# Kernel optimization log

Hardware: AMD Instinct MI355X
Metric: run time of the kernel (lower is better)

## Reference

```python
import jax, jax.numpy as jnp
import numpy as np

B, L, D = 128, 196, 512
T = 20
V, E, H, A = 10000, 256, 512, 512


def setup_inputs() -> dict:
    key = jax.random.key(0)
    ks = jax.random.split(key, 20)
    s = lambda *sh: 0.02
    inp = {
        "a": jax.random.normal(ks[0], (B, L, D), jnp.float32),
        "captions": jax.random.randint(ks[1], (B, T), 0, V),
        "lengths": jnp.full((B,), T, dtype=jnp.int64),
        "embed_W": jax.random.normal(ks[2], (V, E), jnp.float32) * 0.02,
        "Wa": jax.random.normal(ks[3], (D, A), jnp.float32) * 0.02,
        "Wh": jax.random.normal(ks[4], (H, A), jnp.float32) * 0.02,
        "Wc": jax.random.normal(ks[5], (H, A), jnp.float32) * 0.02,
        "v": jax.random.normal(ks[6], (A,), jnp.float32) * 0.02,
        "beta_W": jax.random.normal(ks[7], (H, 1), jnp.float32) * 0.02,
        "beta_b": jnp.zeros((1,), jnp.float32),
        "W_ih": jax.random.normal(ks[8], (E + D, 4 * H), jnp.float32) * 0.02,
        "W_hh": jax.random.normal(ks[9], (H, 4 * H), jnp.float32) * 0.02,
        "b_ih": jnp.zeros((4 * H,), jnp.float32),
        "b_hh": jnp.zeros((4 * H,), jnp.float32),
        "fc_W": jax.random.normal(ks[10], (H, V), jnp.float32) * 0.02,
        "fc_b": jnp.zeros((V,), jnp.float32),
        "initW_h": jax.random.normal(ks[11], (D, H), jnp.float32) * 0.02,
        "initb_h": jnp.zeros((H,), jnp.float32),
        "initW_c": jax.random.normal(ks[12], (D, H), jnp.float32) * 0.02,
        "initb_c": jnp.zeros((H,), jnp.float32),
    }
    return inp


def _decode(a, captions, embed_W, Wa, Wh, Wc, v, beta_W, beta_b,
            W_ih, W_hh, b_ih, b_hh, fc_W, fc_b,
            initW_h, initb_h, initW_c, initb_c):
    # dropout layers are treated as identity (eval mode) for a deterministic reference
    emb = embed_W[captions]                       # (B, T, E)
    mean_ctx = a.mean(axis=1)                     # (B, D)
    h0 = jnp.tanh(mean_ctx @ initW_h + initb_h)   # (B, H)
    c0 = jnp.tanh(mean_ctx @ initW_c + initb_c)
    wa = a @ Wa                                   # (B, L, A), hoisted (invariant over t)
    Hd = h0.shape[-1]

    def step(carry, x_t):
        h, c, prev_h = carry
        # dual additive attention: scores from annotations + h + prev_h (context_input)
        score = jnp.tanh(wa + (h @ Wh)[:, None, :] + (prev_h @ Wc)[:, None, :])  # (B,L,A)
        e = score @ v                                                            # (B,L)
        alpha = jax.nn.softmax(e, axis=1)
        beta = jax.nn.sigmoid(h @ beta_W + beta_b)                               # (B,1)
        ctx = beta * jnp.einsum('bl,bld->bd', alpha, a)                          # (B,D)
        # LSTMCell
        x = jnp.concatenate([x_t, ctx], axis=1)                                  # (B,E+D)
        gates = x @ W_ih + b_ih + h @ W_hh + b_hh                                # (B,4H)
        i, f, g, o = jnp.split(gates, 4, axis=1)
        c_new = jax.nn.sigmoid(f) * c + jax.nn.sigmoid(i) * jnp.tanh(g)
        h_new = jax.nn.sigmoid(o) * jnp.tanh(c_new)
        logits_t = h_new @ fc_W + fc_b                                           # (B,V)
        return (h_new, c_new, h_new), (logits_t, alpha)

    xs = jnp.swapaxes(emb[:, :T - 1, :], 0, 1)    # (T-1, B, E) time-major
    _, (logits_t, alphas_t) = jax.lax.scan(step, (h0, c0, h0), xs)
    # all lengths == T: pack_padded_sequence(batch_first=True).data is time-major flatten
    packed_logits = logits_t.reshape((T - 1) * a.shape[0], -1)                   # ((T-1)*B, V)
    alphas = jnp.swapaxes(alphas_t, 0, 1)                                        # (B, T-1, L)
    return packed_logits, alphas


def reference(a, captions, lengths, embed_W, Wa, Wh, Wc, v, beta_W, beta_b,
              W_ih, W_hh, b_ih, b_hh, fc_W, fc_b,
              initW_h, initb_h, initW_c, initb_c):
    return _decode(a, captions, embed_W, Wa, Wh, Wc, v, beta_W, beta_b,
                   W_ih, W_hh, b_ih, b_hh, fc_W, fc_b,
                   initW_h, initb_h, initW_c, initb_c)
```

## Files before the change

kernel.cpp:

```cpp
#include <hip/hip_runtime.h>
#include <hip/hip_bf16.h>
#include <math.h>

#define B_ 128
#define L_ 196
#define D_ 512
#define T_ 20
#define V_ 10000
#define E_ 256
#define H_ 512
#define A_ 512
#define TM1 19
#define ROWS (TM1*B_)
#define G4H 2048
#define KCAT 1024
#define LH 98

typedef unsigned short ushort_t;
typedef __attribute__((ext_vector_type(8))) short bf16x8;
typedef __attribute__((ext_vector_type(4))) float f32x4;

__device__ __forceinline__ float fast_tanh(float x){
    float ax = fabsf(x);
    float e = __expf(-2.f*ax);
    float r = __builtin_amdgcn_rcpf(1.f + e);
    return copysignf((1.f - e)*r, x);
}
__device__ __forceinline__ float sigmoidf_(float x){
    return __builtin_amdgcn_rcpf(1.f + __expf(-x));
}
__device__ __forceinline__ ushort_t f2b(float f){
    union{float f; unsigned u;} x; x.f = f;
    unsigned r = x.u + 0x7fffu + ((x.u>>16)&1u);
    return (ushort_t)(r>>16);
}
__device__ __forceinline__ float b2f(ushort_t h){
    union{unsigned u; float f;} x; x.u = ((unsigned)h)<<16;
    return x.f;
}
__device__ __forceinline__ float b2f_lo(unsigned u){ union{unsigned u; float f;} x; x.u = u<<16; return x.f; }
__device__ __forceinline__ float b2f_hi(unsigned u){ union{unsigned u; float f;} x; x.u = u & 0xffff0000u; return x.f; }

template<int OUT_BF16, int HAS_BIAS, int NT, int SWZ>
__global__ __launch_bounds__(256)
void gemm_mfma(const ushort_t* __restrict__ A, int lda,
               const ushort_t* __restrict__ BT, int ldb,
               void* __restrict__ Cout, int ldc,
               int N, int K, const float* __restrict__ bias)
{
// ... 135 lines not shown
struct TJob { const float* src; const float* src2; ushort_t* dst;
              int lds, Ksz, Nsz, koff, ldk, nx, nblk; };
struct TJobs { TJob j[6]; };

__global__ __launch_bounds__(256) void combo_trans_k(TJobs J){
    __shared__ float t[32][33];
    int bid = blockIdx.x;
    int ji = 0;
    while (bid >= J.j[ji].nblk){ bid -= J.j[ji].nblk; ji++; }
    const TJob jb = J.j[ji];
    int n0 = (bid % jb.nx)*32, k0 = (bid / jb.nx)*32;
    int tx = threadIdx.x & 31, ty = threadIdx.x >> 5;
    #pragma unroll
    for (int kk = ty; kk < 32; kk += 8){
        int k = k0 + kk, n = n0 + tx;
        float v = 0.f;
        if (k < jb.Ksz && n < jb.Nsz){
            v = jb.src[(size_t)k*jb.lds + n];
            if (jb.src2) v += jb.src2[(size_t)k*jb.lds + n];
        }
        t[kk][tx] = v;
    }
    __syncthreads();
    #pragma unroll
    for (int nn = ty; nn < 32; nn += 8){
        int n = n0 + nn, k = k0 + tx;
        if (k < jb.Ksz) jb.dst[(size_t)n*jb.ldk + jb.koff + k] = f2b(t[tx][nn]);
    }
}

__global__ __launch_bounds__(256) void mean_cvt_k(const float* __restrict__ a, ushort_t* __restrict__ a_b,
                                                  float* __restrict__ mc,
                                                  const float* __restrict__ b_ih, const float* __restrict__ b_hh,
                                                  float* __restrict__ bias4h, unsigned* __restrict__ ebar){
    if (blockIdx.x == 256){
        for (int k = threadIdx.x; k < G4H; k += 256) bias4h[k] = b_ih[k] + b_hh[k];
        if (threadIdx.x < B_) ebar[threadIdx.x] = 0u;
        return;
    }
    int idx = blockIdx.x*256 + threadIdx.x;
    int b = idx >> 9, d = idx & 511;
    const float* p = a + (size_t)b*L_*D_ + d;
    ushort_t* q = a_b + (size_t)b*L_*D_ + d;
    float s = 0.f;
    for (int l=0;l<L_;l++){ float v = p[(size_t)l*D_]; s += v; q[(size_t)l*D_] = f2b(v); }
    mc[idx] = s * (1.f/(float)L_);
}

__global__ void gather_emb(const int* __restrict__ captions, const float* __restrict__ embW,
                           ushort_t* __restrict__ xemb){
    int i = blockIdx.x;
    int t = i / B_, b = i - t*B_;
    int cap = captions[b*T_ + t];
    float4 v = ((const float4*)(embW + (size_t)cap*E_))[threadIdx.x];
    ushort_t r[4] = {f2b(v.x),f2b(v.y),f2b(v.z),f2b(v.w)};
    *(uint2*)(xemb + (size_t)i*E_ + threadIdx.x*4) = *(uint2*)r;
}

__global__ __launch_bounds__(512) void hw0cvt_k(const float* __restrict__ h0f,
                        const ushort_t* __restrict__ WhcT,
                        ushort_t* __restrict__ xcat, float* __restrict__ hWp){
    int b = blockIdx.x, tid = threadIdx.x;
    int lane = tid & 63, wave = tid >> 6;
    __shared__ ushort_t hls[512];
    float hv = h0f[b*H_ + tid];
    ushort_t hb = f2b(hv);
    xcat[(size_t)b*KCAT + D_ + tid] = hb;
    hls[tid] = hb;
    hWp[(size_t)(b*2+1)*512 + tid] = 0.f;
    __syncthreads();
    int wn = wave * 64;
    int col16 = lane & 15;
    int khi = (lane >> 4) * 8;
    bool a_on = (col16 == 0);
    f32x4 acc[4];
    #pragma unroll
    for (int f=0;f<4;f++) acc[f] = (f32x4){0.f,0.f,0.f,0.f};
    for (int kk=0; kk<16; kk++){
        bf16x8 af = (bf16x8){0,0,0,0,0,0,0,0};
        if (a_on) af = *(const bf16x8*)&hls[kk*32 + khi];
        #pragma unroll
        for (int f=0;f<4;f++){
            bf16x8 bf = *(const bf16x8*)(WhcT + (size_t)(wn + f*16 + col16)*512 + kk*32 + khi);
            acc[f] = __builtin_amdgcn_mfma_f32_16x16x32_bf16(af, bf, acc[f], 0, 0, 0);
        }
    }
    if (lane < 16){
        #pragma unroll
        for (int f=0;f<4;f++) hWp[(size_t)(b*2+0)*512 + wn + f*16 + lane] = acc[f][0];
    }
}

__global__ __launch_bounds__(512) void mega2_k(const ushort_t* __restrict__ wa,
                        const ushort_t* __restrict__ a_b,
                        const float* __restrict__ v,
                        const float* __restrict__ beta_W, const float* __restrict__ beta_b,
                        const ushort_t* __restrict__ WhcT,
                        const float* __restrict__ gp, const float* __restrict__ embWih,
                        float* __restrict__ cbuf, float* __restrict__ hWp,
                        ushort_t* __restrict__ xcat, ushort_t* __restrict__ Hall,
                        float* __restrict__ alphas_out, float* __restrict__ ebuf,
                        unsigned* __restrict__ ebar, int t)
{
    const int b = blockIdx.x, half = blockIdx.y;
    const int tid = threadIdx.x;
    const int lane = tid & 63, wave = tid >> 6;
    __shared__ ushort_t hls[256];
    __shared__ float red[512];
    __shared__ float al_s[224];
    __shared__ float part[2][256];

    if (t > 0){
        if (tid < 256){
            const int j = half*256 + tid;
            const float* eb = embWih + ((size_t)((t-1)*B_ + b))*G4H;
            float gi = eb[j], gf = eb[H_+j], gg = eb[2*H_+j], go = eb[3*H_+j];
            #pragma unroll
            for (int ks=0; ks<8; ks++){
                const float* g = gp + ((size_t)(ks*B_ + b))*G4H;
                gi += g[j]; gf += g[H_+j]; gg += g[2*H_+j]; go += g[3*H_+j];
            }
            float ig = sigmoidf_(gi), fg = sigmoidf_(gf);
            float g2 = fast_tanh(gg), og = sigmoidf_(go);
            float c = fg*cbuf[b*H_+j] + ig*g2;
            float h = og*fast_tanh(c);
            cbuf[b*H_+j] = c;
            ushort_t hb = f2b(h);
            xcat[(size_t)b*KCAT + D_ + j] = hb;
            Hall[((size_t)(t-1)*B_ + b)*H_ + j] = hb;
            hls[tid] = hb;
        }
        __syncthreads();
        int wn = wave * 64;
        int col16 = lane & 15;
        int khi = (lane >> 4) * 8;
        bool a_on = (col16 == 0);
        f32x4 acc[4];
        #pragma unroll
        for (int f=0;f<4;f++) acc[f] = (f32x4){0.f,0.f,0.f,0.f};
        #pragma unroll
        for (int kk=0; kk<8; kk++){
            bf16x8 af = (bf16x8){0,0,0,0,0,0,0,0};
            if (a_on) af = *(const bf16x8*)&hls[kk*32 + khi];
            #pragma unroll
            for (int f=0;f<4;f++){
                bf16x8 bf = *(const bf16x8*)(WhcT + (size_t)(wn + f*16 + col16)*512 + half*256 + kk*32 + khi);
                acc[f] = __builtin_amdgcn_mfma_f32_16x16x32_bf16(af, bf, acc[f], 0, 0, 0);
            }
        }
        if (lane < 16){
            #pragma unroll
            for (int f=0;f<4;f++) hWp[(size_t)(b*2+half)*512 + wn + f*16 + lane] = acc[f][0];
        }
    }
    __syncthreads();
    if (tid == 0){
        __threadfence();
        atomicAdd(&ebar[b], 1u);
        const unsigned tgt = 2u*(unsigned)(2*t+1);
        while (__hip_atomic_load(&ebar[b], __ATOMIC_ACQUIRE, __HIP_MEMORY_SCOPE_AGENT) < tgt)
            __builtin_amdgcn_s_sleep(1);
    }
    __syncthreads();
    {
        const float* hp0 = hWp + (size_t)(b*2+0)*512 + lane*8;
        const float* hp1 = hWp + (size_t)(b*2+1)*512 + lane*8;
        float4 p00 = *(const float4*)hp0, p01 = *(const float4*)(hp0+4);
        float4 p10 = *(const float4*)hp1, p11 = *(const float4*)(hp1+4);
        float4 hw0 = make_float4(p00.x+p10.x, p00.y+p10.y, p00.z+p10.z, p00.w+p10.w);
        float4 hw1 = make_float4(p01.x+p11.x, p01.y+p11.y, p01.z+p11.z, p01.w+p11.w);
        const float* vp = v + lane*8;
        float4 v0 = *(const float4*)vp, v1 = *(const float4*)(vp+4);
        const int l0 = half*LH;
        for (int r = wave; r < LH; r += 8){
            int4 raw = *(const int4*)(wa + (((size_t)(b*L_ + l0 + r))<<9) + lane*8);
            const unsigned* u = (const unsigned*)&raw;
            float s;
            s  = fast_tanh(b2f_lo(u[0]) + hw0.x)*v0.x;
            s += fast_tanh(b2f_hi(u[0]) + hw0.y)*v0.y;
            s += fast_tanh(b2f_lo(u[1]) + hw0.z)*v0.z;
            s += fast_tanh(b2f_hi(u[1]) + hw0.w)*v0.w;
            s += fast_tanh(b2f_lo(u[2]) + hw1.x)*v1.x;
            s += fast_tanh(b2f_hi(u[2]) + hw1.y)*v1.y;
            s += fast_tanh(b2f_lo(u[3]) + hw1.z)*v1.z;
            s += fast_tanh(b2f_hi(u[3]) + hw1.w)*v1.w;
            #pragma unroll
            for (int off=32; off; off>>=1) s += __shfl_down(s, off);
            if (lane==0) ebuf[b*L_ + l0 + r] = s;
        }
    }
    __syncthreads();
    if (tid == 0){
        __threadfence();
        atomicAdd(&ebar[b], 1u);
        const unsigned tgt = 2u*(unsigned)(2*t+2);
        while (__hip_atomic_load(&ebar[b], __ATOMIC_ACQUIRE, __HIP_MEMORY_SCOPE_AGENT) < tgt)
            __builtin_amdgcn_s_sleep(1);
    }
    __syncthreads();
    float ev = (tid < L_) ? ebuf[b*L_ + tid] : -3.0e38f;
    red[tid] = ev; __syncthreads();
    #pragma unroll
    for (int s=256; s; s>>=1){ if (tid<s) red[tid] = fmaxf(red[tid], red[tid+s]); __syncthreads(); }
    float m = red[0]; __syncthreads();
    float pr = (tid < L_) ? __expf(ev - m) : 0.f;
    red[tid] = pr; __syncthreads();
    #pragma unroll
    for (int s=256; s; s>>=1){ if (tid<s) red[tid] += red[tid+s]; __syncthreads(); }
    float inv = 1.f / red[0];
    __syncthreads();
    if (tid < L_) al_s[tid] = pr*inv;
    const int l0 = half*LH;
    if (tid >= l0 && tid < l0 + LH)
        __builtin_nontemporal_store(pr*inv, alphas_out + (size_t)b*TM1*L_ + (size_t)t*L_ + tid);
    float dv = b2f(xcat[(size_t)b*KCAT + D_ + tid]) * beta_W[tid];
    red[tid] = dv; __syncthreads();
    #pragma unroll
    for (int s=256; s; s>>=1){ if (tid<s) red[tid] += red[tid+s]; __syncthreads(); }
    float beta = sigmoidf_(red[0] + beta_b[0]);
    __syncthreads();
    const int d  = half*256 + (tid & 255);
    const int lr = tid >> 8;
    const ushort_t* pa = a_b + (((size_t)(b*L_ + lr*LH))<<9) + d;
    float s0 = 0.f;
    #pragma unroll 7
    for (int i=0; i<LH; ++i) s0 = fmaf(al_s[lr*LH + i], b2f(pa[(size_t)i*512]), s0);
    part[lr][tid & 255] = s0;
    __syncthreads();
    if (tid < 256)
        xcat[(size_t)b*KCAT + half*256 + tid] = f2b(beta*(part[0][tid] + part[1][tid]));
}

__global__ __launch_bounds__(256) void gates_k(const ushort_t* __restrict__ xcat,
                        const ushort_t* __restrict__ WcatT, float* __restrict__ gp){
    __shared__ ushort_t As[128*32];
    __shared__ ushort_t Bs[64*32];
    const int bn = blockIdx.x*64;
    const int ks = blockIdx.y;
    const int tid = threadIdx.x;
    const int lane = tid & 63, wave = tid >> 6;
    const int wm = wave*32;
    const int lrow = lane & 15;
    const int lk8 = (lane >> 4) * 8;
    f32x4 acc[2][4];
    #pragma unroll
    for (int i=0;i<2;i++)
        #pragma unroll
        for (int j=0;j<4;j++) acc[i][j] = (f32x4){0.f,0.f,0.f,0.f};

    for (int kk = 0; kk < 4; ++kk){
        int k0 = ks*128 + kk*32;
        int c0 = 2*tid;
        int r0 = c0 >> 2,  kq0 = (c0 & 3)*8;
        int r1 = (c0+1) >> 2, kq1 = ((c0+1) & 3)*8;
        int4 a0 = *(const int4*)(xcat + (size_t)r0*KCAT + k0 + kq0);
        int4 a1 = *(const int4*)(xcat + (size_t)r1*KCAT + k0 + kq1);
        int rb = tid >> 2, kqb = (tid & 3)*8;
        int4 b0 = *(const int4*)(WcatT + (size_t)(bn+rb)*KCAT + k0 + kqb);
        __syncthreads();
        *(int4*)&As[r0*32 + kq0] = a0;
        *(int4*)&As[r1*32 + kq1] = a1;
        *(int4*)&Bs[rb*32 + kqb] = b0;
        __syncthreads();
        bf16x8 af[2], bfr[4];
        #pragma unroll
        for (int i=0;i<2;i++) af[i] = *(bf16x8*)&As[(wm + i*16 + lrow)*32 + lk8];
        #pragma unroll
        for (int j=0;j<4;j++) bfr[j] = *(bf16x8*)&Bs[(j*16 + lrow)*32 + lk8];
        #pragma unroll
        for (int i=0;i<2;i++)
            #pragma unroll
            for (int j=0;j<4;j++)
                acc[i][j] = __builtin_amdgcn_mfma_f32_16x16x32_bf16(af[i], bfr[j], acc[i][j], 0, 0, 0);
    }
    const int rq = (lane >> 4) * 4;
    #pragma unroll
    for (int i=0;i<2;i++){
        #pragma unroll
        for (int j=0;j<4;j++){
            int gcol = bn + j*16 + lrow;
            #pragma unroll
            for (int q=0;q<4;q++){
                int grow = wm + i*16 + rq + q;
                gp[((size_t)(ks*B_ + grow))*G4H + gcol] = acc[i][j][q];
            }
        }
    }
}

__global__ __launch_bounds__(512) void lstmfin_k(const float* __restrict__ gp, const float* __restrict__ embWih,
                       const float* __restrict__ cbuf, ushort_t* __restrict__ Hall){
    int b = blockIdx.x, j = threadIdx.x;
    const float* eb = embWih + ((size_t)(18*B_ + b))*G4H;
    float gi = eb[j], gf = eb[H_+j], gg = eb[2*H_+j], go = eb[3*H_+j];
    #pragma unroll
    for (int ks=0; ks<8; ks++){
        const float* g = gp + ((size_t)(ks*B_ + b))*G4H;
        gi += g[j]; gf += g[H_+j]; gg += g[2*H_+j]; go += g[3*H_+j];
    }
    float ig = sigmoidf_(gi), fg = sigmoidf_(gf);
    float g2 = fast_tanh(gg), og = sigmoidf_(go);
    float c = fg*cbuf[b*H_+j] + ig*g2;
    float h = og*fast_tanh(c);
    Hall[((size_t)18*B_ + b)*H_ + j] = f2b(h);
}

extern "C" void kernel_launch(void* const* d_in, const int* in_sizes, int n_in,
                              void* d_out, int out_size, void* d_ws, size_t ws_size,
                              hipStream_t stream) {
    const float* a      = (const float*)d_in[0];
    const int*   caps   = (const int*)  d_in[1];
    const float* embW   = (const float*)d_in[3];
    const float* Wa     = (const float*)d_in[4];
    const float* Wh     = (const float*)d_in[5];
    const float* Wc     = (const float*)d_in[6];
    const float* v      = (const float*)d_in[7];
    const float* beta_W = (const float*)d_in[8];
    const float* beta_b = (const float*)d_in[9];
    const float* W_ih   = (const float*)d_in[10];
    const float* W_hh   = (const float*)d_in[11];
    const float* b_ih   = (const float*)d_in[12];
    const float* b_hh   = (const float*)d_in[13];
    const float* fc_W   = (const float*)d_in[14];
    const float* fc_b   = (const float*)d_in[15];
    const float* iWh    = (const float*)d_in[16];
    const float* ibh    = (const float*)d_in[17];
    const float* iWc    = (const float*)d_in[18];
    const float* ibc    = (const float*)d_in[19];

    float* out    = (float*)d_out;
    float* alphas = out + (size_t)ROWS*V_;

    char* ob = (char*)d_out;
    ushort_t* wa_b   = (ushort_t*)(ob);
    ushort_t* a_b    = (ushort_t*)(ob + 25690112);
    float*    embWih = (float*)   (ob + 51380224);

    char* wb = (char*)d_ws;
    float* mean_ctx = (float*)(wb);
    float* cbuf     = (float*)(wb + 262144);
    float* h0f      = (float*)(wb + 524288);
    float* hWp      = (float*)(wb + 786432);
    float* ebuf     = (float*)(wb + 1310720);
    float* bias4h   = (float*)(wb + 1413120);
    unsigned* ebar  = (unsigned*)(wb + 1421312);
    float* gp       = (float*)(wb + 1422336);
    ushort_t* xcat_b = (ushort_t*)(wb + 9810944);
    ushort_t* xemb_b = (ushort_t*)(wb + 10073088);
    ushort_t* Hall   = (ushort_t*)(wb + 11318272);
    ushort_t* WaT    = (ushort_t*)(wb + 13808640);
    ushort_t* WhcT   = (ushort_t*)(wb + 14332928);
    ushort_t* WihT   = (ushort_t*)(wb + 14857216);
    ushort_t* WcatT  = (ushort_t*)(wb + 15905792);
    ushort_t* fcWT   = (ushort_t*)(wb + 20100096);

    TJobs J;
    J.j[0] = { Wa,   nullptr, WaT,  512, 512, 512,  0,   512,  16, 256 };
    J.j[1] = { Wh,   Wc,      WhcT, 512, 512, 512,  0,   512,  16, 256 };
    J.j[2] = { W_ih, nullptr, WihT, G4H, 256, G4H,  0,   256,  64, 512 };
    J.j[3] = { W_ih + (size_t)E_*G4H, nullptr, WcatT, G4H, 512, G4H, 0,   KCAT, 64, 1024 };
    J.j[4] = { W_hh, nullptr, WcatT, G4H, 512, G4H,  512, KCAT, 64, 1024 };
    J.j[5] = { fc_W, nullptr, fcWT, V_,  512, V_,   0,   512,  316, 5056 };
    combo_trans_k<<<8128, 256, 0, stream>>>(J);
    mean_cvt_k<<<257, 256, 0, stream>>>(a, a_b, mean_ctx, b_ih, b_hh, bias4h, ebar);
    gather_emb<<<ROWS, 64, 0, stream>>>(caps, embW, xemb_b);
    gemm64t2<<<dim3(8,2,2), 256, 0, stream>>>(mean_ctx, D_, iWh, iWc, H_, h0f, cbuf, H_, ibh, ibc);
    hw0cvt_k<<<B_, 512, 0, stream>>>(h0f, WhcT, xcat_b, hWp);
    gemm_mfma<1,0,0,0><<<dim3(4,196), 256, 0, stream>>>(a_b, D_, WaT, D_, wa_b, A_, A_, D_, nullptr);
    gemm_mfma<0,1,0,0><<<dim3(16,19), 256, 0, stream>>>(xemb_b, E_, WihT, E_, embWih, G4H, G4H, E_, bias4h);

    for (int t = 0; t < TM1; ++t){
        mega2_k<<<dim3(B_,2), 512, 0, stream>>>(wa_b, a_b, v, beta_W, beta_b, WhcT,
                                                gp, embWih, cbuf, hWp, xcat_b, Hall,
                                                alphas, ebuf, ebar, t);
        gates_k<<<dim3(32,8), 256, 0, stream>>>(xcat_b, WcatT, gp);
    }
    lstmfin_k<<<B_, 512, 0, stream>>>(gp, embWih, cbuf, Hall);

    gemm_mfma<0,1,1,1><<<dim3(1520), 256, 0, stream>>>(Hall, H_, fcWT, H_, out, V_, V_, H_, fc_b);
}
```

Before: 1.054 ms.

## Fuse per-timestep attention and gate kernels into one persistent cooperative kernel

Replaces the 19 pairs of per-timestep launches (attention kernel plus gates GEMM) and the final LSTM kernel with a single cooperative persistent kernel of 256 blocks. Timesteps are separated by global atomic spin barriers instead of kernel boundaries. The gates GEMM is retiled to fit 512-thread blocks. This removes about 39 launch gaps and their drain/fill overhead, at the cost of grid-wide barriers with sleep polling and a fixed 256-block residency requirement.

```diff
diff --git a/kernel.cpp b/kernel.cpp
--- a/kernel.cpp
+++ b/kernel.cpp
@@ -15,6 +15,7 @@
 #define G4H 2048
 #define KCAT 1024
 #define LH 98
+#define NBLK 256
 
 typedef unsigned short ushort_t;
 typedef __attribute__((ext_vector_type(8))) short bf16x8;
@@ -216,10 +217,10 @@
 __global__ __launch_bounds__(256) void mean_cvt_k(const float* __restrict__ a, ushort_t* __restrict__ a_b,
                                                   float* __restrict__ mc,
                                                   const float* __restrict__ b_ih, const float* __restrict__ b_hh,
-                                                  float* __restrict__ bias4h, unsigned* __restrict__ ebar){
+                                                  float* __restrict__ bias4h, unsigned* __restrict__ bars){
     if (blockIdx.x == 256){
         for (int k = threadIdx.x; k < G4H; k += 256) bias4h[k] = b_ih[k] + b_hh[k];
-        if (threadIdx.x < B_) ebar[threadIdx.x] = 0u;
+        if (threadIdx.x < B_ + 1) bars[threadIdx.x] = 0u;
         return;
     }
     int idx = blockIdx.x*256 + threadIdx.x;
@@ -275,218 +276,220 @@
     }
 }
 
-__global__ __launch_bounds__(512) void mega2_k(const ushort_t* __restrict__ wa,
-                        const ushort_t* __restrict__ a_b,
-                        const float* __restrict__ v,
-                        const float* __restrict__ beta_W, const float* __restrict__ beta_b,
-                        const ushort_t* __restrict__ WhcT,
-                        const float* __restrict__ gp, const float* __restrict__ embWih,
-                        float* __restrict__ cbuf, float* __restrict__ hWp,
-                        ushort_t* __restrict__ xcat, ushort_t* __restrict__ Hall,
-                        float* __restrict__ alphas_out, float* __restrict__ ebuf,
-                        unsigned* __restrict__ ebar, int t)
-{
-    const int b = blockIdx.x, half = blockIdx.y;
+struct LoopArgs {
+    const ushort_t* wa;
+    const ushort_t* a_b;
+    const float* v;
+    const float* beta_W;
+    const float* beta_b;
+    const ushort_t* WhcT;
+    const ushort_t* WcatT;
+    const float* embWih;
+    float* cbuf;
+    float* hWp;
+    ushort_t* xcat;
+    ushort_t* Hall;
+    float* alphas;
+    float* ebuf;
+    float* gp;
+    unsigned* ebar;
+    unsigned* gbar;
+};
+
+__device__ __forceinline__ void spin_sync(unsigned* ctr, unsigned tgt){
+    __syncthreads();
+    if (threadIdx.x == 0){
+        __threadfence();
+        atomicAdd(ctr, 1u);
+        while (__hip_atomic_load(ctr, __ATOMIC_ACQUIRE, __HIP_MEMORY_SCOPE_AGENT) < tgt)
+            __builtin_amdgcn_s_sleep(1);
+    }
+    __syncthreads();
+}
+
+__global__ __launch_bounds__(512) void loop2_k(LoopArgs p){
+    const int blk = blockIdx.x;
+    const int b = blk >> 1, half = blk & 1;
     const int tid = threadIdx.x;
     const int lane = tid & 63, wave = tid >> 6;
     __shared__ ushort_t hls[256];
     __shared__ float red[512];
     __shared__ float al_s[224];
     __shared__ float part[2][256];
-
-    if (t > 0){
-        if (tid < 256){
-            const int j = half*256 + tid;
-            const float* eb = embWih + ((size_t)((t-1)*B_ + b))*G4H;
-            float gi = eb[j], gf = eb[H_+j], gg = eb[2*H_+j], go = eb[3*H_+j];
-            #pragma unroll
-            for (int ks=0; ks<8; ks++){
-                const float* g = gp + ((size_t)(ks*B_ + b))*G4H;
-                gi += g[j]; gf += g[H_+j]; gg += g[2*H_+j]; go += g[3*H_+j];
-            }
-            float ig = sigmoidf_(gi), fg = sigmoidf_(gf);
-            float g2 = fast_tanh(gg), og = sigmoidf_(go);
-            float c = fg*cbuf[b*H_+j] + ig*g2;
-            float h = og*fast_tanh(c);
-            cbuf[b*H_+j] = c;
-            ushort_t hb = f2b(h);
-            xcat[(size_t)b*KCAT + D_ + j] = hb;
-            Hall[((size_t)(t-1)*B_ + b)*H_ + j] = hb;
-            hls[tid] = hb;
-        }
-        __syncthreads();
-        int wn = wave * 64;
-        int col16 = lane & 15;
-        int khi = (lane >> 4) * 8;
-        bool a_on = (col16 == 0);
-        f32x4 acc[4];
-        #pragma unroll
-        for (int f=0;f<4;f++) acc[f] = (f32x4){0.f,0.f,0.f,0.f};
-        #pragma unroll
-        for (int kk=0; kk<8; kk++){
-            bf16x8 af = (bf16x8){0,0,0,0,0,0,0,0};
-            if (a_on) af = *(const bf16x8*)&hls[kk*32 + khi];
-            #pragma unroll
-            for (int f=0;f<4;f++){
-                bf16x8 bf = *(const bf16x8*)(WhcT + (size_t)(wn + f*16 + col16)*512 + half*256 + kk*32 + khi);
-                acc[f] = __builtin_amdgcn_mfma_f32_16x16x32_bf16(af, bf, acc[f], 0, 0, 0);
-            }
-        }
-        if (lane < 16){
-            #pragma unroll
-            for (int f=0;f<4;f++) hWp[(size_t)(b*2+half)*512 + wn + f*16 + lane] = acc[f][0];
-        }
-    }
-    __syncthreads();
-    if (tid == 0){
-        __threadfence();
-        atomicAdd(&ebar[b], 1u);
-        const unsigned tgt = 2u*(unsigned)(2*t+1);
-        while (__hip_atomic_load(&ebar[b], __ATOMIC_ACQUIRE, __HIP_MEMORY_SCOPE_AGENT) < tgt)
-            __builtin_amdgcn_s_sleep(1);
-    }
-    __syncthreads();
-    {
-        const float* hp0 = hWp + (size_t)(b*2+0)*512 + lane*8;
-        const float* hp1 = hWp + (size_t)(b*2+1)*512 + lane*8;
-        float4 p00 = *(const float4*)hp0, p01 = *(const float4*)(hp0+4);
-        float4 p10 = *(const float4*)hp1, p11 = *(const float4*)(hp1+4);
-        float4 hw0 = make_float4(p00.x+p10.x, p00.y+p10.y, p00.z+p10.z, p00.w+p10.w);
-        float4 hw1 = make_float4(p01.x+p11.x, p01.y+p11.y, p01.z+p11.z, p01.w+p11.w);
-        const float* vp = v + lane*8;
-        float4 v0 = *(const float4*)vp, v1 = *(const float4*)(vp+4);
-        const int l0 = half*LH;
-        for (int r = wave; r < LH; r += 8){
-            int4 raw = *(const int4*)(wa + (((size_t)(b*L_ + l0 + r))<<9) + lane*8);
-            const unsigned* u = (const unsigned*)&raw;
-            float s;
-            s  = fast_tanh(b2f_lo(u[0]) + hw0.x)*v0.x;
-            s += fast_tanh(b2f_hi(u[0]) + hw0.y)*v0.y;
-            s += fast_tanh(b2f_lo(u[1]) + hw0.z)*v0.z;
-            s += fast_tanh(b2f_hi(u[1]) + hw0.w)*v0.w;
-            s += fast_tanh(b2f_lo(u[2]) + hw1.x)*v1.x;
-            s += fast_tanh(b2f_hi(u[2]) + hw1.y)*v1.y;
-            s += fast_tanh(b2f_lo(u[3]) + hw1.z)*v1.z;
-            s += fast_tanh(b2f_hi(u[3]) + hw1.w)*v1.w;
-            #pragma unroll
-            for (int off=32; off; off>>=1) s += __shfl_down(s, off);
-            if (lane==0) ebuf[b*L_ + l0 + r] = s;
-        }
-    }
-    __syncthreads();
-    if (tid == 0){
-        __threadfence();
-        atomicAdd(&ebar[b], 1u);
-        const unsigned tgt = 2u*(unsigned)(2*t+2);
-        while (__hip_atomic_load(&ebar[b], __ATOMIC_ACQUIRE, __HIP_MEMORY_SCOPE_AGENT) < tgt)
-            __builtin_amdgcn_s_sleep(1);
-    }
-    __syncthreads();
-    float ev = (tid < L_) ? ebuf[b*L_ + tid] : -3.0e38f;
-    red[tid] = ev; __syncthreads();
-    #pragma unroll
-    for (int s=256; s; s>>=1){ if (tid<s) red[tid] = fmaxf(red[tid], red[tid+s]); __syncthreads(); }
-    float m = red[0]; __syncthreads();
-    float pr = (tid < L_) ? __expf(ev - m) : 0.f;
-    red[tid] = pr; __syncthreads();
-    #pragma unroll
-    for (int s=256; s; s>>=1){ if (tid<s) red[tid] += red[tid+s]; __syncthreads(); }
-    float inv = 1.f / red[0];
-    __syncthreads();
-    if (tid < L_) al_s[tid] = pr*inv;
-    const int l0 = half*LH;
-    if (tid >= l0 && tid < l0 + LH)
-        __builtin_nontemporal_store(pr*inv, alphas_out + (size_t)b*TM1*L_ + (size_t)t*L_ + tid);
-    float dv = b2f(xcat[(size_t)b*KCAT + D_ + tid]) * beta_W[tid];
-    red[tid] = dv; __syncthreads();
-    #pragma unroll
-    for (int s=256; s; s>>=1){ if (tid<s) red[tid] += red[tid+s]; __syncthreads(); }
-    float beta = sigmoidf_(red[0] + beta_b[0]);
-    __syncthreads();
-    const int d  = half*256 + (tid & 255);
-    const int lr = tid >> 8;
-    const ushort_t* pa = a_b + (((size_t)(b*L_ + lr*LH))<<9) + d;
-    float s0 = 0.f;
-    #pragma unroll 7
-    for (int i=0; i<LH; ++i) s0 = fmaf(al_s[lr*LH + i], b2f(pa[(size_t)i*512]), s0);
-    part[lr][tid & 255] = s0;
-    __syncthreads();
-    if (tid < 256)
-        xcat[(size_t)b*KCAT + half*256 + tid] = f2b(beta*(part[0][tid] + part[1][tid]));
-}
-
-__global__ __launch_bounds__(256) void gates_k(const ushort_t* __restrict__ xcat,
-                        const ushort_t* __restrict__ WcatT, float* __restrict__ gp){
     __shared__ ushort_t As[128*32];
     __shared__ ushort_t Bs[64*32];
-    const int bn = blockIdx.x*64;
-    const int ks = blockIdx.y;
-    const int tid = threadIdx.x;
-    const int lane = tid & 63, wave = tid >> 6;
-    const int wm = wave*32;
-    const int lrow = lane & 15;
-    const int lk8 = (lane >> 4) * 8;
-    f32x4 acc[2][4];
-    #pragma unroll
-    for (int i=0;i<2;i++)
-        #pragma unroll
-        for (int j=0;j<4;j++) acc[i][j] = (f32x4){0.f,0.f,0.f,0.f};
-
-    for (int kk = 0; kk < 4; ++kk){
-        int k0 = ks*128 + kk*32;
-        int c0 = 2*tid;
-        int r0 = c0 >> 2,  kq0 = (c0 & 3)*8;
-        int r1 = (c0+1) >> 2, kq1 = ((c0+1) & 3)*8;
-        int4 a0 = *(const int4*)(xcat + (size_t)r0*KCAT + k0 + kq0);
-        int4 a1 = *(const int4*)(xcat + (size_t)r1*KCAT + k0 + kq1);
-        int rb = tid >> 2, kqb = (tid & 3)*8;
-        int4 b0 = *(const int4*)(WcatT + (size_t)(bn+rb)*KCAT + k0 + kqb);
-        __syncthreads();
-        *(int4*)&As[r0*32 + kq0] = a0;
-        *(int4*)&As[r1*32 + kq1] = a1;
-        *(int4*)&Bs[rb*32 + kqb] = b0;
-        __syncthreads();
-        bf16x8 af[2], bfr[4];
-        #pragma unroll
-        for (int i=0;i<2;i++) af[i] = *(bf16x8*)&As[(wm + i*16 + lrow)*32 + lk8];
-        #pragma unroll
-        for (int j=0;j<4;j++) bfr[j] = *(bf16x8*)&Bs[(j*16 + lrow)*32 + lk8];
-        #pragma unroll
-        for (int i=0;i<2;i++)
-            #pragma unroll
-            for (int j=0;j<4;j++)
-                acc[i][j] = __builtin_amdgcn_mfma_f32_16x16x32_bf16(af[i], bfr[j], acc[i][j], 0, 0, 0);
-    }
-    const int rq = (lane >> 4) * 4;
-    #pragma unroll
-    for (int i=0;i<2;i++){
-        #pragma unroll
-        for (int j=0;j<4;j++){
-            int gcol = bn + j*16 + lrow;
-            #pragma unroll
-            for (int q=0;q<4;q++){
-                int grow = wm + i*16 + rq + q;
-                gp[((size_t)(ks*B_ + grow))*G4H + gcol] = acc[i][j][q];
+    unsigned gtgt = 0;
+
+    for (int t = 0; t < TM1; ++t){
+        if (t > 0){
+            if (tid < 256){
+                const int j = half*256 + tid;
+                const float* eb = p.embWih + ((size_t)((t-1)*B_ + b))*G4H;
+                float gi = eb[j], gf = eb[H_+j], gg = eb[2*H_+j], go = eb[3*H_+j];
+                #pragma unroll
+                for (int ks=0; ks<8; ks++){
+                    const float* g = p.gp + ((size_t)(ks*B_ + b))*G4H;
+                    gi += g[j]; gf += g[H_+j]; gg += g[2*H_+j]; go += g[3*H_+j];
+                }
+                float ig = sigmoidf_(gi), fg = sigmoidf_(gf);
+                float g2 = fast_tanh(gg), og = sigmoidf_(go);
+                float c = fg*p.cbuf[b*H_+j] + ig*g2;
+                float h = og*fast_tanh(c);
+                p.cbuf[b*H_+j] = c;
+                ushort_t hb = f2b(h);
+                p.xcat[(size_t)b*KCAT + D_ + j] = hb;
+                p.Hall[((size_t)(t-1)*B_ + b)*H_ + j] = hb;
+                hls[tid] = hb;
             }
-        }
-    }
-}
-
-__global__ __launch_bounds__(512) void lstmfin_k(const float* __restrict__ gp, const float* __restrict__ embWih,
-                       const float* __restrict__ cbuf, ushort_t* __restrict__ Hall){
-    int b = blockIdx.x, j = threadIdx.x;
-    const float* eb = embWih + ((size_t)(18*B_ + b))*G4H;
-    float gi = eb[j], gf = eb[H_+j], gg = eb[2*H_+j], go = eb[3*H_+j];
-    #pragma unroll
-    for (int ks=0; ks<8; ks++){
-        const float* g = gp + ((size_t)(ks*B_ + b))*G4H;
-        gi += g[j]; gf += g[H_+j]; gg += g[2*H_+j]; go += g[3*H_+j];
-    }
-    float ig = sigmoidf_(gi), fg = sigmoidf_(gf);
-    float g2 = fast_tanh(gg), og = sigmoidf_(go);
-    float c = fg*cbuf[b*H_+j] + ig*g2;
-    float h = og*fast_tanh(c);
-    Hall[((size_t)18*B_ + b)*H_ + j] = f2b(h);
+            __syncthreads();
+            int wn = wave * 64;
+            int col16 = lane & 15;
+            int khi = (lane >> 4) * 8;
+            bool a_on = (col16 == 0);
+            f32x4 acc[4];
+            #pragma unroll
+            for (int f=0;f<4;f++) acc[f] = (f32x4){0.f,0.f,0.f,0.f};
+            #pragma unroll
+            for (int kk=0; kk<8; kk++){
+                bf16x8 af = (bf16x8){0,0,0,0,0,0,0,0};
+                if (a_on) af = *(const bf16x8*)&hls[kk*32 + khi];
+                #pragma unroll
+                for (int f=0;f<4;f++){
+                    bf16x8 bf = *(const bf16x8*)(p.WhcT + (size_t)(wn + f*16 + col16)*512 + half*256 + kk*32 + khi);
+                    acc[f] = __builtin_amdgcn_mfma_f32_16x16x32_bf16(af, bf, acc[f], 0, 0, 0);
+                }
+            }
+            if (lane < 16){
+                #pragma unroll
+                for (int f=0;f<4;f++) p.hWp[(size_t)(b*2+half)*512 + wn + f*16 + lane] = acc[f][0];
+            }
+        }
+        spin_sync(&p.ebar[b], 4u*(unsigned)t + 2u);
+        {
+            const float* hp0 = p.hWp + (size_t)(b*2+0)*512 + lane*8;
+            const float* hp1 = p.hWp + (size_t)(b*2+1)*512 + lane*8;
+            float4 p00 = *(const float4*)hp0, p01 = *(const float4*)(hp0+4);
+            float4 p10 = *(const float4*)hp1, p11 = *(const float4*)(hp1+4);
+            float4 hw0 = make_float4(p00.x+p10.x, p00.y+p10.y, p00.z+p10.z, p00.w+p10.w);
+            float4 hw1 = make_float4(p01.x+p11.x, p01.y+p11.y, p01.z+p11.z, p01.w+p11.w);
+            const float* vp = p.v + lane*8;
+            float4 v0 = *(const float4*)vp, v1 = *(const float4*)(vp+4);
+            const int l0 = half*LH;
+            for (int r = wave; r < LH; r += 8){
+                int4 raw = *(const int4*)(p.wa + (((size_t)(b*L_ + l0 + r))<<9) + lane*8);
+                const unsigned* u = (const unsigned*)&raw;
+                float s;
+                s  = fast_tanh(b2f_lo(u[0]) + hw0.x)*v0.x;
+                s += fast_tanh(b2f_hi(u[0]) + hw0.y)*v0.y;
+                s += fast_tanh(b2f_lo(u[1]) + hw0.z)*v0.z;
+                s += fast_tanh(b2f_hi(u[1]) + hw0.w)*v0.w;
+                s += fast_tanh(b2f_lo(u[2]) + hw1.x)*v1.x;
+                s += fast_tanh(b2f_hi(u[2]) + hw1.y)*v1.y;
+                s += fast_tanh(b2f_lo(u[3]) + hw1.z)*v1.z;
+                s += fast_tanh(b2f_hi(u[3]) + hw1.w)*v1.w;
+                #pragma unroll
+                for (int off=32; off; off>>=1) s += __shfl_down(s, off);
+                if (lane==0) p.ebuf[b*L_ + l0 + r] = s;
+            }
+        }
+        spin_sync(&p.ebar[b], 4u*(unsigned)t + 4u);
+        {
+            float ev = (tid < L_) ? p.ebuf[b*L_ + tid] : -3.0e38f;
+            red[tid] = ev; __syncthreads();
+            #pragma unroll
+            for (int s=256; s; s>>=1){ if (tid<s) red[tid] = fmaxf(red[tid], red[tid+s]); __syncthreads(); }
+            float m = red[0]; __syncthreads();
+            float pr = (tid < L_) ? __expf(ev - m) : 0.f;
+            red[tid] = pr; __syncthreads();
+            #pragma unroll
+            for (int s=256; s; s>>=1){ if (tid<s) red[tid] += red[tid+s]; __syncthreads(); }
+            float inv = 1.f / red[0];
+            __syncthreads();
+            if (tid < L_) al_s[tid] = pr*inv;
+            const int l0 = half*LH;
+            if (tid >= l0 && tid < l0 + LH)
+                __builtin_nontemporal_store(pr*inv, p.alphas + (size_t)b*TM1*L_ + (size_t)t*L_ + tid);
+            float dv = b2f(p.xcat[(size_t)b*KCAT + D_ + tid]) * p.beta_W[tid];
+            red[tid] = dv; __syncthreads();
+            #pragma unroll
+            for (int s=256; s; s>>=1){ if (tid<s) red[tid] += red[tid+s]; __syncthreads(); }
+            float beta = sigmoidf_(red[0] + p.beta_b[0]);
+            __syncthreads();
+            const int d  = half*256 + (tid & 255);
+            const int lr = tid >> 8;
+            const ushort_t* pa = p.a_b + (((size_t)(b*L_ + lr*LH))<<9) + d;
+            float s0 = 0.f;
+            #pragma unroll 7
+            for (int i=0; i<LH; ++i) s0 = fmaf(al_s[lr*LH + i], b2f(pa[(size_t)i*512]), s0);
+            part[lr][tid & 255] = s0;
+            __syncthreads();
+            if (tid < 256)
+                p.xcat[(size_t)b*KCAT + half*256 + tid] = f2b(beta*(part[0][tid] + part[1][tid]));
+        }
+        gtgt += NBLK; spin_sync(p.gbar, gtgt);
+        {
+            const int bn = (blk & 31) * 64;
+            const int ks = blk >> 5;
+            const int wm = (wave & 3) * 32;
+            const int wn = (wave >> 2) * 32;
+            const int lrow = lane & 15, lk8 = (lane >> 4) * 8;
+            const int ra = tid >> 2, kqa = (tid & 3)*8;
+            f32x4 acc[2][2];
+            #pragma unroll
+            for (int i=0;i<2;i++)
+                #pragma unroll
+                for (int j=0;j<2;j++) acc[i][j] = (f32x4){0.f,0.f,0.f,0.f};
+            #pragma unroll
+            for (int kk = 0; kk < 4; ++kk){
+                int k0 = ks*128 + kk*32;
+                int4 av = *(const int4*)(p.xcat + (size_t)ra*KCAT + k0 + kqa);
+                int4 bv;
+                if (tid < 256) bv = *(const int4*)(p.WcatT + (size_t)(bn + ra)*KCAT + k0 + kqa);
+                __syncthreads();
+                *(int4*)&As[ra*32 + kqa] = av;
+                if (tid < 256) *(int4*)&Bs[ra*32 + kqa] = bv;
+                __syncthreads();
+                bf16x8 af[2], bfr[2];
+                #pragma unroll
+                for (int i=0;i<2;i++) af[i]  = *(bf16x8*)&As[(wm + i*16 + lrow)*32 + lk8];
+                #pragma unroll
+                for (int j=0;j<2;j++) bfr[j] = *(bf16x8*)&Bs[(wn + j*16 + lrow)*32 + lk8];
+                #pragma unroll
+                for (int i=0;i<2;i++)
+                    #pragma unroll
+                    for (int j=0;j<2;j++)
+                        acc[i][j] = __builtin_amdgcn_mfma_f32_16x16x32_bf16(af[i], bfr[j], acc[i][j], 0, 0, 0);
+            }
+            const int rq = (lane >> 4) * 4;
+            #pragma unroll
+            for (int i=0;i<2;i++)
+                #pragma unroll
+                for (int j=0;j<2;j++){
+                    int gcol = bn + wn + j*16 + lrow;
+                    #pragma unroll
+                    for (int q=0;q<4;q++){
+                        int grow = wm + i*16 + rq + q;
+                        p.gp[((size_t)(ks*B_ + grow))*G4H + gcol] = acc[i][j][q];
+                    }
+                }
+        }
+        gtgt += NBLK; spin_sync(p.gbar, gtgt);
+    }
+    if (tid < 256){
+        const int j = half*256 + tid;
+        const float* eb = p.embWih + ((size_t)(18*B_ + b))*G4H;
+        float gi = eb[j], gf = eb[H_+j], gg = eb[2*H_+j], go = eb[3*H_+j];
+        #pragma unroll
+        for (int ks=0; ks<8; ks++){
+            const float* g = p.gp + ((size_t)(ks*B_ + b))*G4H;
+            gi += g[j]; gf += g[H_+j]; gg += g[2*H_+j]; go += g[3*H_+j];
+        }
+        float ig = sigmoidf_(gi), fg = sigmoidf_(gf);
+        float g2 = fast_tanh(gg), og = sigmoidf_(go);
+        float c = fg*p.cbuf[b*H_+j] + ig*g2;
+        float h = og*fast_tanh(c);
+        p.Hall[((size_t)18*B_ + b)*H_ + j] = f2b(h);
+    }
 }
 
 extern "C" void kernel_launch(void* const* d_in, const int* in_sizes, int n_in,
@@ -527,7 +530,7 @@
     float* hWp      = (float*)(wb + 786432);
     float* ebuf     = (float*)(wb + 1310720);
     float* bias4h   = (float*)(wb + 1413120);
-    unsigned* ebar  = (unsigned*)(wb + 1421312);
+    unsigned* bars  = (unsigned*)(wb + 1421312);
     float* gp       = (float*)(wb + 1422336);
     ushort_t* xcat_b = (ushort_t*)(wb + 9810944);
     ushort_t* xemb_b = (ushort_t*)(wb + 10073088);
@@ -546,20 +549,21 @@
     J.j[4] = { W_hh, nullptr, WcatT, G4H, 512, G4H,  512, KCAT, 64, 1024 };
     J.j[5] = { fc_W, nullptr, fcWT, V_,  512, V_,   0,   512,  316, 5056 };
     combo_trans_k<<<8128, 256, 0, stream>>>(J);
-    mean_cvt_k<<<257, 256, 0, stream>>>(a, a_b, mean_ctx, b_ih, b_hh, bias4h, ebar);
+    mean_cvt_k<<<257, 256, 0, stream>>>(a, a_b, mean_ctx, b_ih, b_hh, bias4h, bars);
     gather_emb<<<ROWS, 64, 0, stream>>>(caps, embW, xemb_b);
     gemm64t2<<<dim3(8,2,2), 256, 0, stream>>>(mean_ctx, D_, iWh, iWc, H_, h0f, cbuf, H_, ibh, ibc);
     hw0cvt_k<<<B_, 512, 0, stream>>>(h0f, WhcT, xcat_b, hWp);
     gemm_mfma<1,0,0,0><<<dim3(4,196), 256, 0, stream>>>(a_b, D_, WaT, D_, wa_b, A_, A_, D_, nullptr);
     gemm_mfma<0,1,0,0><<<dim3(16,19), 256, 0, stream>>>(xemb_b, E_, WihT, E_, embWih, G4H, G4H, E_, bias4h);
 
-    for (int t = 0; t < TM1; ++t){
-        mega2_k<<<dim3(B_,2), 512, 0, stream>>>(wa_b, a_b, v, beta_W, beta_b, WhcT,
-                                                gp, embWih, cbuf, hWp, xcat_b, Hall,
-                                                alphas, ebuf, ebar, t);
-        gates_k<<<dim3(32,8), 256, 0, stream>>>(xcat_b, WcatT, gp);
-    }
-    lstmfin_k<<<B_, 512, 0, stream>>>(gp, embWih, cbuf, Hall);
+    LoopArgs la;
+    la.wa = wa_b; la.a_b = a_b; la.v = v; la.beta_W = beta_W; la.beta_b = beta_b;
+    la.WhcT = WhcT; la.WcatT = WcatT; la.embWih = embWih;
+    la.cbuf = cbuf; la.hWp = hWp; la.xcat = xcat_b; la.Hall = Hall;
+    la.alphas = alphas; la.ebuf = ebuf; la.gp = gp;
+    la.ebar = bars; la.gbar = bars + 128;
+    void* kargs[] = { &la };
+    hipLaunchCooperativeKernel((const void*)loop2_k, dim3(NBLK), dim3(512), kargs, 0, stream);
 
     gemm_mfma<0,1,1,1><<<dim3(1520), 256, 0, stream>>>(Hall, H_, fcWT, H_, out, V_, V_, H_, fc_b);
 }
```

Result: slower. 2.202 ms (+108.8%).

## Split per-step attention kernel into four quarter blocks per batch row

Applied to the files above, without the earlier changes.

The per-timestep attention/LSTM-cell kernel now runs as 4 blocks of 256 threads per batch element instead of 2 blocks of 512. The hW partial products are kept in four slices and summed after a cross-block spin barrier, which is factored into a helper, and the score rows and context columns are divided into quarters. Separately, mean_cvt is vectorized with float4 loads and gather_emb packs four rows per block. The aim is more, smaller blocks for better CU occupancy on the latency-bound recurrent loop, at the cost of more blocks spinning on each per-batch barrier and more redundant softmax/beta work.

```diff
diff --git a/kernel.cpp b/kernel.cpp
--- a/kernel.cpp
+++ b/kernel.cpp
@@ -14,7 +14,7 @@
 #define ROWS (TM1*B_)
 #define G4H 2048
 #define KCAT 1024
-#define LH 98
+#define LQ 49
 
 typedef unsigned short ushort_t;
 typedef __attribute__((ext_vector_type(8))) short bf16x8;
@@ -216,29 +216,37 @@
 __global__ __launch_bounds__(256) void mean_cvt_k(const float* __restrict__ a, ushort_t* __restrict__ a_b,
                                                   float* __restrict__ mc,
                                                   const float* __restrict__ b_ih, const float* __restrict__ b_hh,
-                                                  float* __restrict__ bias4h, unsigned* __restrict__ ebar){
-    if (blockIdx.x == 256){
+                                                  float* __restrict__ bias4h, unsigned* __restrict__ bars){
+    if (blockIdx.x == 64){
         for (int k = threadIdx.x; k < G4H; k += 256) bias4h[k] = b_ih[k] + b_hh[k];
-        if (threadIdx.x < B_) ebar[threadIdx.x] = 0u;
+        if (threadIdx.x < B_) bars[threadIdx.x] = 0u;
         return;
     }
     int idx = blockIdx.x*256 + threadIdx.x;
-    int b = idx >> 9, d = idx & 511;
-    const float* p = a + (size_t)b*L_*D_ + d;
-    ushort_t* q = a_b + (size_t)b*L_*D_ + d;
-    float s = 0.f;
-    for (int l=0;l<L_;l++){ float v = p[(size_t)l*D_]; s += v; q[(size_t)l*D_] = f2b(v); }
-    mc[idx] = s * (1.f/(float)L_);
-}
-
-__global__ void gather_emb(const int* __restrict__ captions, const float* __restrict__ embW,
+    int b = idx >> 7, dq = (idx & 127) * 4;
+    const float* p = a + (size_t)b*L_*D_ + dq;
+    ushort_t* q = a_b + (size_t)b*L_*D_ + dq;
+    float4 s = make_float4(0.f,0.f,0.f,0.f);
+    for (int l=0;l<L_;l++){
+        float4 v = *(const float4*)(p + (size_t)l*D_);
+        s.x += v.x; s.y += v.y; s.z += v.z; s.w += v.w;
+        ushort_t r[4] = {f2b(v.x),f2b(v.y),f2b(v.z),f2b(v.w)};
+        *(uint2*)(q + (size_t)l*D_) = *(uint2*)r;
+    }
+    const float inv = 1.f/(float)L_;
+    float4 o = make_float4(s.x*inv, s.y*inv, s.z*inv, s.w*inv);
+    *(float4*)(mc + (size_t)b*D_ + dq) = o;
+}
+
+__global__ __launch_bounds__(256) void gather_emb(const int* __restrict__ captions, const float* __restrict__ embW,
                            ushort_t* __restrict__ xemb){
-    int i = blockIdx.x;
+    int i = blockIdx.x*4 + (threadIdx.x >> 6);
+    int lane = threadIdx.x & 63;
     int t = i / B_, b = i - t*B_;
     int cap = captions[b*T_ + t];
-    float4 v = ((const float4*)(embW + (size_t)cap*E_))[threadIdx.x];
+    float4 v = ((const float4*)(embW + (size_t)cap*E_))[lane];
     ushort_t r[4] = {f2b(v.x),f2b(v.y),f2b(v.z),f2b(v.w)};
-    *(uint2*)(xemb + (size_t)i*E_ + threadIdx.x*4) = *(uint2*)r;
+    *(uint2*)(xemb + (size_t)i*E_ + lane*4) = *(uint2*)r;
 }
 
 __global__ __launch_bounds__(512) void hw0cvt_k(const float* __restrict__ h0f,
@@ -251,7 +259,9 @@
     ushort_t hb = f2b(hv);
     xcat[(size_t)b*KCAT + D_ + tid] = hb;
     hls[tid] = hb;
-    hWp[(size_t)(b*2+1)*512 + tid] = 0.f;
+    hWp[(size_t)(b*4+1)*512 + tid] = 0.f;
+    hWp[(size_t)(b*4+2)*512 + tid] = 0.f;
+    hWp[(size_t)(b*4+3)*512 + tid] = 0.f;
     __syncthreads();
     int wn = wave * 64;
     int col16 = lane & 15;
@@ -271,11 +281,22 @@
     }
     if (lane < 16){
         #pragma unroll
-        for (int f=0;f<4;f++) hWp[(size_t)(b*2+0)*512 + wn + f*16 + lane] = acc[f][0];
-    }
-}
-
-__global__ __launch_bounds__(512) void mega2_k(const ushort_t* __restrict__ wa,
+        for (int f=0;f<4;f++) hWp[(size_t)(b*4+0)*512 + wn + f*16 + lane] = acc[f][0];
+    }
+}
+
+__device__ __forceinline__ void spin_sync(unsigned* ctr, unsigned tgt){
+    __syncthreads();
+    if (threadIdx.x == 0){
+        __threadfence();
+        atomicAdd(ctr, 1u);
+        while (__hip_atomic_load(ctr, __ATOMIC_ACQUIRE, __HIP_MEMORY_SCOPE_AGENT) < tgt)
+            __builtin_amdgcn_s_sleep(1);
+    }
+    __syncthreads();
+}
+
+__global__ __launch_bounds__(256) void mega3_k(const ushort_t* __restrict__ wa,
                         const ushort_t* __restrict__ a_b,
                         const float* __restrict__ v,
                         const float* __restrict__ beta_W, const float* __restrict__ beta_b,
@@ -286,17 +307,17 @@
                         float* __restrict__ alphas_out, float* __restrict__ ebuf,
                         unsigned* __restrict__ ebar, int t)
 {
-    const int b = blockIdx.x, half = blockIdx.y;
+    const int b = blockIdx.x, q = blockIdx.y;
     const int tid = threadIdx.x;
     const int lane = tid & 63, wave = tid >> 6;
-    __shared__ ushort_t hls[256];
-    __shared__ float red[512];
+    __shared__ ushort_t hls[128];
+    __shared__ float red[256];
     __shared__ float al_s[224];
-    __shared__ float part[2][256];
+    __shared__ float part[2][128];
 
     if (t > 0){
-        if (tid < 256){
-            const int j = half*256 + tid;
+        if (tid < 128){
+            const int j = q*128 + tid;
             const float* eb = embWih + ((size_t)((t-1)*B_ + b))*G4H;
             float gi = eb[j], gf = eb[H_+j], gg = eb[2*H_+j], go = eb[3*H_+j];
             #pragma unroll
@@ -315,48 +336,43 @@
             hls[tid] = hb;
         }
         __syncthreads();
-        int wn = wave * 64;
-        int col16 = lane & 15;
-        int khi = (lane >> 4) * 8;
-        bool a_on = (col16 == 0);
-        f32x4 acc[4];
-        #pragma unroll
-        for (int f=0;f<4;f++) acc[f] = (f32x4){0.f,0.f,0.f,0.f};
-        #pragma unroll
-        for (int kk=0; kk<8; kk++){
+        const int col16 = lane & 15;
+        const int khi = (lane >> 4) * 8;
+        const bool a_on = (col16 == 0);
+        f32x4 acc[8];
+        #pragma unroll
+        for (int f=0;f<8;f++) acc[f] = (f32x4){0.f,0.f,0.f,0.f};
+        #pragma unroll
+        for (int kk=0; kk<4; kk++){
             bf16x8 af = (bf16x8){0,0,0,0,0,0,0,0};
             if (a_on) af = *(const bf16x8*)&hls[kk*32 + khi];
             #pragma unroll
-            for (int f=0;f<4;f++){
-                bf16x8 bf = *(const bf16x8*)(WhcT + (size_t)(wn + f*16 + col16)*512 + half*256 + kk*32 + khi);
+            for (int f=0;f<8;f++){
+                int col = wave*128 + f*16 + col16;
+                bf16x8 bf = *(const bf16x8*)(WhcT + (size_t)col*512 + q*128 + kk*32 + khi);
                 acc[f] = __builtin_amdgcn_mfma_f32_16x16x32_bf16(af, bf, acc[f], 0, 0, 0);
             }
         }
         if (lane < 16){
             #pragma unroll
-            for (int f=0;f<4;f++) hWp[(size_t)(b*2+half)*512 + wn + f*16 + lane] = acc[f][0];
-        }
-    }
-    __syncthreads();
-    if (tid == 0){
-        __threadfence();
-        atomicAdd(&ebar[b], 1u);
-        const unsigned tgt = 2u*(unsigned)(2*t+1);
-        while (__hip_atomic_load(&ebar[b], __ATOMIC_ACQUIRE, __HIP_MEMORY_SCOPE_AGENT) < tgt)
-            __builtin_amdgcn_s_sleep(1);
-    }
-    __syncthreads();
+            for (int f=0;f<8;f++)
+                hWp[(size_t)(b*4+q)*512 + wave*128 + f*16 + lane] = acc[f][0];
+        }
+    }
+    spin_sync(&ebar[b], 8u*(unsigned)t + 4u);
     {
-        const float* hp0 = hWp + (size_t)(b*2+0)*512 + lane*8;
-        const float* hp1 = hWp + (size_t)(b*2+1)*512 + lane*8;
-        float4 p00 = *(const float4*)hp0, p01 = *(const float4*)(hp0+4);
-        float4 p10 = *(const float4*)hp1, p11 = *(const float4*)(hp1+4);
-        float4 hw0 = make_float4(p00.x+p10.x, p00.y+p10.y, p00.z+p10.z, p00.w+p10.w);
-        float4 hw1 = make_float4(p01.x+p11.x, p01.y+p11.y, p01.z+p11.z, p01.w+p11.w);
+        float4 hw0 = make_float4(0.f,0.f,0.f,0.f), hw1 = make_float4(0.f,0.f,0.f,0.f);
+        #pragma unroll
+        for (int qq=0; qq<4; qq++){
+            const float* hp = hWp + (size_t)(b*4+qq)*512 + lane*8;
+            float4 x0 = *(const float4*)hp, x1 = *(const float4*)(hp+4);
+            hw0.x += x0.x; hw0.y += x0.y; hw0.z += x0.z; hw0.w += x0.w;
+            hw1.x += x1.x; hw1.y += x1.y; hw1.z += x1.z; hw1.w += x1.w;
+        }
         const float* vp = v + lane*8;
         float4 v0 = *(const float4*)vp, v1 = *(const float4*)(vp+4);
-        const int l0 = half*LH;
-        for (int r = wave; r < LH; r += 8){
+        const int l0 = q*LQ;
+        for (int r = wave; r < LQ; r += 4){
             int4 raw = *(const int4*)(wa + (((size_t)(b*L_ + l0 + r))<<9) + lane*8);
             const unsigned* u = (const unsigned*)&raw;
             float s;
@@ -373,46 +389,41 @@
             if (lane==0) ebuf[b*L_ + l0 + r] = s;
         }
     }
-    __syncthreads();
-    if (tid == 0){
-        __threadfence();
-        atomicAdd(&ebar[b], 1u);
-        const unsigned tgt = 2u*(unsigned)(2*t+2);
-        while (__hip_atomic_load(&ebar[b], __ATOMIC_ACQUIRE, __HIP_MEMORY_SCOPE_AGENT) < tgt)
-            __builtin_amdgcn_s_sleep(1);
-    }
-    __syncthreads();
+    spin_sync(&ebar[b], 8u*(unsigned)t + 8u);
     float ev = (tid < L_) ? ebuf[b*L_ + tid] : -3.0e38f;
     red[tid] = ev; __syncthreads();
     #pragma unroll
-    for (int s=256; s; s>>=1){ if (tid<s) red[tid] = fmaxf(red[tid], red[tid+s]); __syncthreads(); }
+    for (int s=128; s; s>>=1){ if (tid<s) red[tid] = fmaxf(red[tid], red[tid+s]); __syncthreads(); }
     float m = red[0]; __syncthreads();
     float pr = (tid < L_) ? __expf(ev - m) : 0.f;
     red[tid] = pr; __syncthreads();
     #pragma unroll
-    for (int s=256; s; s>>=1){ if (tid<s) red[tid] += red[tid+s]; __syncthreads(); }
+    for (int s=128; s; s>>=1){ if (tid<s) red[tid] += red[tid+s]; __syncthreads(); }
     float inv = 1.f / red[0];
     __syncthreads();
     if (tid < L_) al_s[tid] = pr*inv;
-    const int l0 = half*LH;
-    if (tid >= l0 && tid < l0 + LH)
+    if (tid >= q*LQ && tid < q*LQ + LQ)
         __builtin_nontemporal_store(pr*inv, alphas_out + (size_t)b*TM1*L_ + (size_t)t*L_ + tid);
-    float dv = b2f(xcat[(size_t)b*KCAT + D_ + tid]) * beta_W[tid];
-    red[tid] = dv; __syncthreads();
-    #pragma unroll
-    for (int s=256; s; s>>=1){ if (tid<s) red[tid] += red[tid+s]; __syncthreads(); }
+    {
+        const ushort_t* hb = xcat + (size_t)b*KCAT + D_;
+        float dv = b2f(hb[tid])*beta_W[tid] + b2f(hb[tid+256])*beta_W[tid+256];
+        red[tid] = dv;
+    }
+    __syncthreads();
+    #pragma unroll
+    for (int s=128; s; s>>=1){ if (tid<s) red[tid] += red[tid+s]; __syncthreads(); }
     float beta = sigmoidf_(red[0] + beta_b[0]);
     __syncthreads();
-    const int d  = half*256 + (tid & 255);
-    const int lr = tid >> 8;
-    const ushort_t* pa = a_b + (((size_t)(b*L_ + lr*LH))<<9) + d;
+    const int d  = q*128 + (tid & 127);
+    const int lr = tid >> 7;
+    const ushort_t* pa = a_b + (((size_t)(b*L_ + lr*98))<<9) + d;
     float s0 = 0.f;
     #pragma unroll 7
-    for (int i=0; i<LH; ++i) s0 = fmaf(al_s[lr*LH + i], b2f(pa[(size_t)i*512]), s0);
-    part[lr][tid & 255] = s0;
-    __syncthreads();
-    if (tid < 256)
-        xcat[(size_t)b*KCAT + half*256 + tid] = f2b(beta*(part[0][tid] + part[1][tid]));
+    for (int i=0; i<98; ++i) s0 = fmaf(al_s[lr*98 + i], b2f(pa[(size_t)i*512]), s0);
+    part[lr][tid & 127] = s0;
+    __syncthreads();
+    if (tid < 128)
+        xcat[(size_t)b*KCAT + q*128 + tid] = f2b(beta*(part[0][tid] + part[1][tid]));
 }
 
 __global__ __launch_bounds__(256) void gates_k(const ushort_t* __restrict__ xcat,
@@ -525,18 +536,18 @@
     float* cbuf     = (float*)(wb + 262144);
     float* h0f      = (float*)(wb + 524288);
     float* hWp      = (float*)(wb + 786432);
-    float* ebuf     = (float*)(wb + 1310720);
-    float* bias4h   = (float*)(wb + 1413120);
-    unsigned* ebar  = (unsigned*)(wb + 1421312);
-    float* gp       = (float*)(wb + 1422336);
-    ushort_t* xcat_b = (ushort_t*)(wb + 9810944);
-    ushort_t* xemb_b = (ushort_t*)(wb + 10073088);
-    ushort_t* Hall   = (ushort_t*)(wb + 11318272);
-    ushort_t* WaT    = (ushort_t*)(wb + 13808640);
-    ushort_t* WhcT   = (ushort_t*)(wb + 14332928);
-    ushort_t* WihT   = (ushort_t*)(wb + 14857216);
-    ushort_t* WcatT  = (ushort_t*)(wb + 15905792);
-    ushort_t* fcWT   = (ushort_t*)(wb + 20100096);
+    float* ebuf     = (float*)(wb + 1835008);
+    float* bias4h   = (float*)(wb + 1937408);
+    unsigned* bars  = (unsigned*)(wb + 1945600);
+    float* gp       = (float*)(wb + 1949696);
+    ushort_t* xcat_b = (ushort_t*)(wb + 10338304);
+    ushort_t* xemb_b = (ushort_t*)(wb + 10600448);
+    ushort_t* Hall   = (ushort_t*)(wb + 11845632);
+    ushort_t* WaT    = (ushort_t*)(wb + 14336000);
+    ushort_t* WhcT   = (ushort_t*)(wb + 14860288);
+    ushort_t* WihT   = (ushort_t*)(wb + 15384576);
+    ushort_t* WcatT  = (ushort_t*)(wb + 16433152);
+    ushort_t* fcWT   = (ushort_t*)(wb + 20627456);
 
     TJobs J;
     J.j[0] = { Wa,   nullptr, WaT,  512, 512, 512,  0,   512,  16, 256 };
@@ -546,17 +557,17 @@
     J.j[4] = { W_hh, nullptr, WcatT, G4H, 512, G4H,  512, KCAT, 64, 1024 };
     J.j[5] = { fc_W, nullptr, fcWT, V_,  512, V_,   0,   512,  316, 5056 };
     combo_trans_k<<<8128, 256, 0, stream>>>(J);
-    mean_cvt_k<<<257, 256, 0, stream>>>(a, a_b, mean_ctx, b_ih, b_hh, bias4h, ebar);
-    gather_emb<<<ROWS, 64, 0, stream>>>(caps, embW, xemb_b);
+    mean_cvt_k<<<65, 256, 0, stream>>>(a, a_b, mean_ctx, b_ih, b_hh, bias4h, bars);
+    gather_emb<<<ROWS/4, 256, 0, stream>>>(caps, embW, xemb_b);
     gemm64t2<<<dim3(8,2,2), 256, 0, stream>>>(mean_ctx, D_, iWh, iWc, H_, h0f, cbuf, H_, ibh, ibc);
     hw0cvt_k<<<B_, 512, 0, stream>>>(h0f, WhcT, xcat_b, hWp);
     gemm_mfma<1,0,0,0><<<dim3(4,196), 256, 0, stream>>>(a_b, D_, WaT, D_, wa_b, A_, A_, D_, nullptr);
     gemm_mfma<0,1,0,0><<<dim3(16,19), 256, 0, stream>>>(xemb_b, E_, WihT, E_, embWih, G4H, G4H, E_, bias4h);
 
     for (int t = 0; t < TM1; ++t){
-        mega2_k<<<dim3(B_,2), 512, 0, stream>>>(wa_b, a_b, v, beta_W, beta_b, WhcT,
+        mega3_k<<<dim3(B_,4), 256, 0, stream>>>(wa_b, a_b, v, beta_W, beta_b, WhcT,
                                                 gp, embWih, cbuf, hWp, xcat_b, Hall,
-                                                alphas, ebuf, ebar, t);
+                                                alphas, ebuf, bars, t);
         gates_k<<<dim3(32,8), 256, 0, stream>>>(xcat_b, WcatT, gp);
     }
     lstmfin_k<<<B_, 512, 0, stream>>>(gp, embWih, cbuf, Hall);
```

After: 1.485 ms. +40.9%, slower.
